# Performance work log

Hardware: AMD Instinct MI355X
Metric: run time of the kernel (lower is better)

Reference implementation:

```python
import jax, jax.numpy as jnp
import numpy as np

N = 50_000          # num_nodes
E = 800_000         # num_edges (avg degree 16)
DIMS = [512, 256, 256, 7]   # embedding_dim
SCALING = 2.0


def _glorot(key, shape):
    lim = float(np.sqrt(6.0 / (shape[0] + shape[1])))
    return jax.random.uniform(key, shape, jnp.float32, -lim, lim)


def setup_inputs() -> dict:
    key = jax.random.key(0)
    ks = jax.random.split(key, 16)
    inp = {
        "x": jax.random.normal(ks[0], (N, DIMS[0]), jnp.float32),
        "edge_index": jax.random.randint(ks[1], (2, E), 0, N, dtype=jnp.int32),
        # GCNConv weights (3 layers)
        "W1": _glorot(ks[2], (DIMS[0], DIMS[1])), "b1": jnp.zeros((DIMS[1],), jnp.float32),
        "W2": _glorot(ks[3], (DIMS[1], DIMS[2])), "b2": jnp.zeros((DIMS[2],), jnp.float32),
        "W3": _glorot(ks[4], (DIMS[2], DIMS[3])), "b3": jnp.zeros((DIMS[3],), jnp.float32),
        # pseudo_mlp: Linear(512,512) -> ReLU -> Linear(512,64) -> ReLU -> Linear(64,out)
        "mw1": _glorot(ks[5], (DIMS[0], 512)), "mb1": jnp.zeros((512,), jnp.float32),
        "mw2": _glorot(ks[6], (512, 64)),      "mb2": jnp.zeros((64,), jnp.float32),
        "mw3": _glorot(ks[7], (64, DIMS[-1])), "mb3": jnp.zeros((DIMS[-1],), jnp.float32),
        # parsing_mats[0] (only index 0 is used: learn_soft_edge3 always called with ln=0)
        "parsing0": jnp.ones((DIMS[-1], DIMS[-1]), jnp.float32) / SCALING,
    }
    return inp


def _gcn_conv(h_in, row, col, edge_weight, W, b):
    """PyG-style GCNConv with self-loops, symmetric norm, and per-edge weights."""
    h = h_in @ W                                  # [N, out]
    loop = jnp.arange(N, dtype=row.dtype)
    r = jnp.concatenate([row, loop])
    c = jnp.concatenate([col, loop])
    ew = jnp.concatenate([edge_weight, jnp.ones((N,), h.dtype)])
    deg = jax.ops.segment_sum(ew, c, num_segments=N)
    dinv = jnp.where(deg > 0, jax.lax.rsqrt(jnp.maximum(deg, 1e-12)), 0.0)
    norm = dinv[r] * ew * dinv[c]                 # [E+N]
    out = jax.ops.segment_sum(h[r] * norm[:, None], c, num_segments=N)
    return out + b


def _learn_soft_edge(x, row, col, mw1, mb1, mw2, mb2, mw3, mb3, parsing0):
    # pseudo_mlp logits
    h = jax.nn.relu(x @ mw1 + mb1)
    h = jax.nn.relu(h @ mw2 + mb2)
    logits = h @ mw3 + mb3                        # [N, C]
    s = logits[row]                               # start_logits [E, C]
    e = logits[col]                               # end_logits   [E, C]
    parsing = jax.nn.relu(SCALING * parsing0)     # [C, C]
    # diag(bmm(outer(s,e), P)).sum(-1) == sum_{c,d} s[e,c] * e[e,d] * P[d,c]
    ew = jnp.sum(s * (e @ parsing), axis=1)       # [E]
    mean = ew.mean()
    var = ew.var(ddof=1)                          # torch .var() is unbiased
    return (ew - mean) * jnp.sqrt(1e-4 / var) + 1.0


def reference(x, edge_index, W1, b1, W2, b2, W3, b3,
              mw1, mb1, mw2, mb2, mw3, mb3, parsing0):
    row, col = edge_index[0], edge_index[1]
    ew = _learn_soft_edge(x, row, col, mw1, mb1, mw2, mb2, mw3, mb3, parsing0)
    # layer 0
    h0 = _gcn_conv(x, row, col, ew, W1, b1)       # h = x (saved, pre-ReLU)
    x1 = jax.nn.relu(h0)                          # dropout is identity in eval
    # layer 1 (+ residual to h0)
    x2 = _gcn_conv(x1, row, col, ew, W2, b2)
    x2 = jax.nn.relu(x2) + h0
    # layer 2 (final, no activation)
    out = _gcn_conv(x2, row, col, ew, W3, b3)     # [N, n_classes]
    return out
```

## Files before the change

### kernel.cpp

```cpp
#include <hip/hip_runtime.h>

#define NN 50000
#define EE 800000
#define NB_EDGE 3125
#define NB_E1   1563
#define NB_SCAN 196

typedef __attribute__((ext_vector_type(4))) float f32x4;
typedef __attribute__((ext_vector_type(8))) short bf16x8;
typedef __attribute__((ext_vector_type(8))) unsigned short u16x8;

typedef const __attribute__((address_space(1))) void* gas_p;
typedef __attribute__((address_space(3))) void* las_p;

__device__ __forceinline__ float bf2f(unsigned short u) {
  union { unsigned int i; float f; } v; v.i = ((unsigned int)u) << 16; return v.f;
}
__device__ __forceinline__ unsigned short f2bf(float f) {
  union { float f; unsigned int i; } v; v.f = f;
  unsigned int u = v.i;
  return (unsigned short)((u + 0x7FFFu + ((u >> 16) & 1u)) >> 16);
}

__device__ __forceinline__ int xcd_swizzle(int orig, int nwg) {
  int xcd = orig & 7;
  int pos = orig >> 3;
  int q = nwg >> 3, r = nwg & 7;
  return (xcd < r ? xcd * (q + 1) : r * (q + 1) + (xcd - r) * q) + pos;
}

constexpr size_t O_XBF  = 0;
constexpr size_t O_H1   = O_XBF + 51200000;
constexpr size_t O_G1   = O_H1  + 51200000;
constexpr size_t O_X1   = O_G1  + 25600000;
constexpr size_t O_H2   = O_X1  + 25600000;
constexpr size_t O_LG   = O_H2  + 6400000;
constexpr size_t O_TG   = O_LG  + 1600000;
constexpr size_t O_EWR  = O_TG  + 1600000;
constexpr size_t O_EWS  = O_EWR + 3200000;
constexpr size_t O_CSR  = O_EWS + 3200000;
constexpr size_t O_MW1T = O_CSR + 6400000;
constexpr size_t O_W1T  = O_MW1T + 524288;
constexpr size_t O_W2T  = O_W1T  + 262144;
constexpr size_t O_MW2T = O_W2T  + 131072;
constexpr size_t O_DEG  = O_MW2T + 65536;
constexpr size_t O_CNT  = O_DEG  + 200192;
constexpr size_t O_CUR  = O_CNT  + 200192;
constexpr size_t O_RED  = O_CUR  + 200192;
constexpr size_t O_RPT  = O_RED  + 256;
constexpr size_t O_DINV = O_RPT  + 200192;
constexpr size_t O_BSUM = O_DINV + 200192;

__global__ __launch_bounds__(256) void conv_f2bf4(const float* __restrict__ in,
                                                  unsigned short* __restrict__ out, int n4) {
  int i = blockIdx.x * 256 + threadIdx.x;
  if (i >= n4) return;
  const float4 v = ((const float4*)in)[i];
  ushort4 o; o.x = f2bf(v.x); o.y = f2bf(v.y); o.z = f2bf(v.z); o.w = f2bf(v.w);
  ((ushort4*)out)[i] = o;
}

__global__ __launch_bounds__(256)
void conv_weights(const float* __restrict__ mw1, const float* __restrict__ W1,
                  const float* __restrict__ W2, const float* __restrict__ mw2,
                  unsigned short* __restrict__ mw1t, unsigned short* __restrict__ w1t,
                  unsigned short* __restrict__ w2t, unsigned short* __restrict__ mw2t)
{
  int i = blockIdx.x * 256 + threadIdx.x;
  if (i < 262144) {
    int k = i >> 9, n = i & 511;
    mw1t[(size_t)n * 512 + k] = f2bf(mw1[i]);
  } else if (i < 393216) {
    int j = i - 262144, k = j >> 8, n = j & 255;
    w1t[(size_t)n * 512 + k] = f2bf(W1[j]);
  } else if (i < 458752) {
    int j = i - 393216, k = j >> 8, n = j & 255;
    w2t[(size_t)n * 256 + k] = f2bf(W2[j]);
  } else if (i < 491520) {
    int j = i - 458752, k = j >> 6, n = j & 63;
    mw2t[(size_t)n * 512 + k] = f2bf(mw2[j]);
  }
}

#define GEMM_STAGE(buf, k0)                                                        \
  _Pragma("unroll")                                                                \
  for (int r = 0; r < 4; ++r) {                                                    \
    const int row = r * 32 + wid * 8 + srow8;                                      \
    int ga = bm + row; ga = ga < M_ ? ga : M_ - 1;                                 \
    int gb = bn + row; gb = gb < N_ ? gb : N_ - 1;                                 \
    __builtin_amdgcn_global_load_lds((gas_p)(pA_ + ((size_t)ga * lda_ + (k0)) * 2 + sks * 16), \
                                     (las_p)(ldsA[buf] + row * 64), 16, 0, 0);     \
    __builtin_amdgcn_global_load_lds((gas_p)(pB_ + ((size_t)gb * ldb_ + (k0)) * 2 + sks * 16), \
                                     (las_p)(ldsB[buf] + row * 64), 16, 0, 0);     \
  }

#define GEMM_BODY(A, lda, Bt, ldb_K, M, Ncols, K, bm, bn)                          \
  __shared__ unsigned short ldsA[2][128 * 64];                                     \
  __shared__ unsigned short ldsB[2][128 * 64];                                     \
  const char* pA_ = (const char*)(A);                                              \
  const char* pB_ = (const char*)(Bt);                                             \
  const int lda_ = (lda), ldb_ = (ldb_K), M_ = (M), N_ = (Ncols);                  \
  const int tid  = threadIdx.x;                                                    \
  const int lane = tid & 63;                                                       \
  const int wid  = tid >> 6;                                                       \
  const int wm   = (wid >> 1) << 6;                                                \
  const int wn   = (wid & 1) << 6;                                                 \
  f32x4 acc[4][4] = {};                                                            \
  const int srow8 = lane >> 3;                                                     \
  const int sks   = (lane & 7) ^ srow8;                                            \
  const int nt    = (K) >> 6;                                                      \
  GEMM_STAGE(0, 0)                                                                 \
  for (int t = 0; t < nt; ++t) {                                                   \
    const int cur = t & 1;                                                         \
    if (t + 1 < nt) {                                                              \
      GEMM_STAGE(cur ^ 1, (t + 1) << 6)                                            \
      asm volatile("s_waitcnt vmcnt(8)" ::: "memory");                             \
    } else {                                                                       \
      asm volatile("s_waitcnt vmcnt(0)" ::: "memory");                             \
    }                                                                              \
    __builtin_amdgcn_s_barrier();                                                  \
    __builtin_amdgcn_sched_barrier(0);                                             \
    const int q   = lane >> 4;                                                     \
    const int r15 = lane & 15;                                                     \
    _Pragma("unroll")                                                              \
    for (int kk = 0; kk < 2; ++kk) {                                               \
      bf16x8 af[4], bfr[4];                                                        \
      _Pragma("unroll")                                                            \
      for (int m = 0; m < 4; ++m) {                                                \
        const int ra = wm + m * 16 + r15;                                          \
        af[m]  = *(const bf16x8*)(ldsA[cur] + ra * 64 + (((kk << 2) + q) ^ (ra & 7)) * 8); \
        const int rb = wn + m * 16 + r15;                                          \
        bfr[m] = *(const bf16x8*)(ldsB[cur] + rb * 64 + (((kk << 2) + q) ^ (rb & 7)) * 8); \
      }                                                                            \
      _Pragma("unroll")                                                            \
      for (int m = 0; m < 4; ++m)                                                  \
        _Pragma("unroll")                                                          \
        for (int n = 0; n < 4; ++n)                                                \
          acc[m][n] = __builtin_amdgcn_mfma_f32_16x16x32_bf16(af[m], bfr[n], acc[m][n], 0, 0, 0); \
    }                                                                              \
    __builtin_amdgcn_sched_barrier(0);                                             \
    __builtin_amdgcn_s_barrier();                                                  \
  }

template<bool RELU, bool BIAS>
__global__ __launch_bounds__(256)
void gemm_bf16(const unsigned short* __restrict__ A, int lda,
               const unsigned short* __restrict__ Bt,
               const float* __restrict__ bias,
               unsigned short* __restrict__ C, int ldc,
               int M, int N, int K)
{
  const int nwg  = gridDim.x * gridDim.y;
  const int wgid = xcd_swizzle(blockIdx.y * gridDim.x + blockIdx.x, nwg);
  const int bn   = (wgid % gridDim.x) << 7;
  const int bm   = (wgid / gridDim.x) << 7;

  GEMM_BODY(A, lda, Bt, K, M, N, K, bm, bn)

  const int q   = lane >> 4;
  const int r15 = lane & 15;
#pragma unroll
  for (int m = 0; m < 4; ++m) {
#pragma unroll
    for (int n = 0; n < 4; ++n) {
      const int gc = bn + wn + n * 16 + r15;
#pragma unroll
      for (int i = 0; i < 4; ++i) {
        const int gr = bm + wm + m * 16 + q * 4 + i;
        if (gr < M && gc < N) {
          float f = acc[m][n][i];
          if (BIAS) f += bias[gc];
          if (RELU) f = fmaxf(f, 0.f);
          C[(size_t)gr * ldc + gc] = f2bf(f);
        }
      }
    }
  }
}

__global__ __launch_bounds__(256)
void gemm_fused(const unsigned short* __restrict__ A,
                const unsigned short* __restrict__ Bt,
                const float* __restrict__ mb1,
                unsigned short* __restrict__ h1,
                unsigned short* __restrict__ g1,
                int M)
{
  const int nwg  = gridDim.x * gridDim.y;
  const int wgid = xcd_swizzle(blockIdx.y * gridDim.x + blockIdx.x, nwg);
  const int bnt  = wgid % gridDim.x;
  const int bn   = bnt << 7;
  const int bm   = (wgid / gridDim.x) << 7;

  GEMM_BODY(A, 512, Bt, 512, M, 768, 512, bm, bn)

  const int q   = lane >> 4;
  const int r15 = lane & 15;
  if (bnt < 4) {
#pragma unroll
    for (int m = 0; m < 4; ++m) {
#pragma unroll
      for (int n = 0; n < 4; ++n) {
        const int gc = bn + wn + n * 16 + r15;
        const float b = mb1[gc];
#pragma unroll
        for (int i = 0; i < 4; ++i) {
          const int gr = bm + wm + m * 16 + q * 4 + i;
          if (gr < M) h1[(size_t)gr * 512 + gc] = f2bf(fmaxf(acc[m][n][i] + b, 0.f));
        }
      }
    }
  } else {
#pragma unroll
    for (int m = 0; m < 4; ++m) {
#pragma unroll
      for (int n = 0; n < 4; ++n) {
        const int gc = bn - 512 + wn + n * 16 + r15;
#pragma unroll
        for (int i = 0; i < 4; ++i) {
          const int gr = bm + wm + m * 16 + q * 4 + i;
          if (gr < M) g1[(size_t)gr * 256 + gc] = f2bf(acc[m][n][i]);
        }
      }
    }
  }
}

__global__ __launch_bounds__(256)
void logits_kernel(const unsigned short* __restrict__ h2, const float* __restrict__ mw3,
                   const float* __restrict__ mb3, const float* __restrict__ par,
                   float* __restrict__ Lg, float* __restrict__ Tg)
{
  __shared__ float w[64 * 8];
  __shared__ float P[64];
  int tid = threadIdx.x;
  for (int i = tid; i < 512; i += 256) {
    int k = i >> 3, c = i & 7;
    w[i] = (c < 7) ? mw3[k * 7 + c] : 0.f;
  }
  if (tid < 64) {
    int d = tid >> 3, c = tid & 7;
    P[tid] = (d < 7 && c < 7) ? fmaxf(2.0f * par[d * 7 + c], 0.f) : 0.f;
  }
  __syncthreads();
  int n = blockIdx.x * 256 + tid;
  if (n >= NN) return;
  const unsigned short* hr = h2 + (size_t)n * 64;
  f32x4 L0 = {0,0,0,0}, L1 = {0,0,0,0};
  for (int k = 0; k < 64; k += 4) {
    ushort4 v = *(const ushort4*)(hr + k);
    float xs[4] = {bf2f(v.x), bf2f(v.y), bf2f(v.z), bf2f(v.w)};
#pragma unroll
    for (int j = 0; j < 4; ++j) {
      L0 += xs[j] * *(const f32x4*)&w[(k + j) * 8];
      L1 += xs[j] * *(const f32x4*)&w[(k + j) * 8 + 4];
    }
  }
  float Ls[8] = {L0[0], L0[1], L0[2], L0[3], L1[0], L1[1], L1[2], 0.f};
#pragma unroll
  for (int c = 0; c < 7; ++c) Ls[c] += mb3[c];
  f32x4 T0 = {0,0,0,0}, T1 = {0,0,0,0};
#pragma unroll
  for (int d = 0; d < 7; ++d) {
    T0 += Ls[d] * *(const f32x4*)&P[d * 8];
    T1 += Ls[d] * *(const f32x4*)&P[d * 8 + 4];
  }
  f32x4 o0 = {Ls[0], Ls[1], Ls[2], Ls[3]};
  f32x4 o1 = {Ls[4], Ls[5], Ls[6], 0.f};
  *(f32x4*)(Lg + (size_t)n * 8)     = o0;
  *(f32x4*)(Lg + (size_t)n * 8 + 4) = o1;
  *(f32x4*)(Tg + (size_t)n * 8)     = T0;
  *(f32x4*)(Tg + (size_t)n * 8 + 4) = T1;
}

__global__ __launch_bounds__(256)
void edge1_kernel(const int* __restrict__ row, const int* __restrict__ col,
                  const float* __restrict__ Lg, const float* __restrict__ Tg,
                  float* __restrict__ ew_raw, int* __restrict__ cnt,
                  double* __restrict__ part)
{
  __shared__ double shs[4], shs2[4];
  const int e0 = blockIdx.x * 512 + threadIdx.x;
  const int e1 = e0 + 256;
  double s = 0.0, s2 = 0.0;
  if (e1 < EE) {
    int r0 = row[e0], c0 = col[e0];
    int r1 = row[e1], c1 = col[e1];
    float4 a00 = *(const float4*)(Lg + (size_t)r0 * 8);
    float4 a01 = *(const float4*)(Lg + (size_t)r0 * 8 + 4);
    float4 a10 = *(const float4*)(Lg + (size_t)r1 * 8);
    float4 a11 = *(const float4*)(Lg + (size_t)r1 * 8 + 4);
    float4 b00 = *(const float4*)(Tg + (size_t)c0 * 8);
    float4 b01 = *(const float4*)(Tg + (size_t)c0 * 8 + 4);
    float4 b10 = *(const float4*)(Tg + (size_t)c1 * 8);
    float4 b11 = *(const float4*)(Tg + (size_t)c1 * 8 + 4);
    float v0 = a00.x*b00.x + a00.y*b00.y + a00.z*b00.z + a00.w*b00.w
             + a01.x*b01.x + a01.y*b01.y + a01.z*b01.z + a01.w*b01.w;
    float v1 = a10.x*b10.x + a10.y*b10.y + a10.z*b10.z + a10.w*b10.w
             + a11.x*b11.x + a11.y*b11.y + a11.z*b11.z + a11.w*b11.w;
    ew_raw[e0] = v0; ew_raw[e1] = v1;
    atomicAdd(&cnt[c0], 1); atomicAdd(&cnt[c1], 1);
    s = (double)v0 + (double)v1;
    s2 = (double)v0 * (double)v0 + (double)v1 * (double)v1;
  } else if (e0 < EE) {
    int r0 = row[e0], c0 = col[e0];
    float4 a00 = *(const float4*)(Lg + (size_t)r0 * 8);
    float4 a01 = *(const float4*)(Lg + (size_t)r0 * 8 + 4);
    float4 b00 = *(const float4*)(Tg + (size_t)c0 * 8);
    float4 b01 = *(const float4*)(Tg + (size_t)c0 * 8 + 4);
    float v0 = a00.x*b00.x + a00.y*b00.y + a00.z*b00.z + a00.w*b00.w
             + a01.x*b01.x + a01.y*b01.y + a01.z*b01.z + a01.w*b01.w;
    ew_raw[e0] = v0;
    atomicAdd(&cnt[c0], 1);
    s = (double)v0; s2 = (double)v0 * (double)v0;
  }
  for (int off = 32; off; off >>= 1) {
    s  += __shfl_down(s, off);
    s2 += __shfl_down(s2, off);
  }
  int wv = threadIdx.x >> 6;
  if ((threadIdx.x & 63) == 0) { shs[wv] = s; shs2[wv] = s2; }
  __syncthreads();
  if (threadIdx.x == 0) {
    part[blockIdx.x]         = shs[0] + shs[1] + shs[2] + shs[3];
    part[NB_E1 + blockIdx.x] = shs2[0] + shs2[1] + shs2[2] + shs2[3];
  }
}

__global__ __launch_bounds__(1024)
void redpart_kernel(const double* __restrict__ part, double* __restrict__ red)
{
  __shared__ double sh[16][2];
  int tid = threadIdx.x;
  double s = 0.0, s2 = 0.0;
  for (int i = tid; i < NB_E1; i += 1024) {
    s  += part[i];
    s2 += part[NB_E1 + i];
  }
  for (int off = 32; off; off >>= 1) {
    s  += __shfl_down(s, off);
    s2 += __shfl_down(s2, off);
  }
  if ((tid & 63) == 0) { sh[tid >> 6][0] = s; sh[tid >> 6][1] = s2; }
  __syncthreads();
  if (tid == 0) {
    double a = 0.0, b = 0.0;
    for (int i = 0; i < 16; ++i) { a += sh[i][0]; b += sh[i][1]; }
    red[0] = a; red[1] = b;
  }
}

__global__ __launch_bounds__(256)
void edge2_kernel(const int* __restrict__ row, const int* __restrict__ col,
                  const float* __restrict__ ew_raw, const double* __restrict__ red,
                  const int* __restrict__ rowptr, int* __restrict__ cursor,
                  float* __restrict__ deg, int2* __restrict__ csr_sw)
{
  int e = blockIdx.x * 256 + threadIdx.x;
  if (e >= EE) return;
  double mean = red[0] / (double)EE;
  double var  = (red[1] - (double)EE * mean * mean) / (double)(EE - 1);
  double scl  = sqrt(1e-4 / var);
  float v = (float)(((double)ew_raw[e] - mean) * scl) + 1.0f;
  int c = col[e];
  atomicAdd(&deg[c], v);
  int pos = atomicAdd(&cursor[c], 1);
  int2 sw; sw.x = row[e]; sw.y = __float_as_int(v);
  csr_sw[rowptr[c] + pos] = sw;
}

__global__ __launch_bounds__(256)
void dinv_kernel(const float* __restrict__ deg, float* __restrict__ dinv)
{
  int n = blockIdx.x * 256 + threadIdx.x;
  if (n >= NN) return;
  float d = deg[n] + 1.0f;
  dinv[n] = d > 0.f ? 1.0f / sqrtf(fmaxf(d, 1e-12f)) : 0.f;
}

__global__ __launch_bounds__(256)
void scan1_kernel(const int* __restrict__ cnt, int* __restrict__ bsum)
{
  __shared__ int sh[4];
  int i = blockIdx.x * 256 + threadIdx.x;
  int v = (i < NN) ? cnt[i] : 0;
  for (int off = 32; off; off >>= 1) v += __shfl_down(v, off);
  if ((threadIdx.x & 63) == 0) sh[threadIdx.x >> 6] = v;
  __syncthreads();
  if (threadIdx.x == 0) bsum[blockIdx.x] = sh[0] + sh[1] + sh[2] + sh[3];
}

__global__ __launch_bounds__(256)
void scan2_kernel(int* __restrict__ bsum)
{
  __shared__ int sh[256];
  int tid = threadIdx.x;
  int v = (tid < NB_SCAN) ? bsum[tid] : 0;
  sh[tid] = v;
  __syncthreads();
  for (int off = 1; off < 256; off <<= 1) {
    int t = (tid >= off) ? sh[tid - off] : 0;
    __syncthreads();
    sh[tid] += t;
    __syncthreads();
  }
  if (tid < NB_SCAN) bsum[tid] = sh[tid] - v;
}

__global__ __launch_bounds__(256)
void scan3_kernel(const int* __restrict__ cnt, const int* __restrict__ bsum,
                  int* __restrict__ rowptr)
{
  __shared__ int sh[256];
  int tid = threadIdx.x;
  int i = blockIdx.x * 256 + tid;
  int v = (i < NN) ? cnt[i] : 0;
  sh[tid] = v;
  __syncthreads();
  for (int off = 1; off < 256; off <<= 1) {
    int t = (tid >= off) ? sh[tid - off] : 0;
    __syncthreads();
    sh[tid] += t;
    __syncthreads();
  }
  if (i < NN) rowptr[i + 1] = bsum[blockIdx.x] + sh[tid];
  if (i == 0) rowptr[0] = 0;
}

#define AGG_ACC(sw_, v_, dv_)                                                \
  {                                                                          \
    float w_ = __int_as_float((sw_).y) * (dv_);                              \
    a0 += w_ * bf2f((v_)[0]); a1 += w_ * bf2f((v_)[1]);                      \
    a2 += w_ * bf2f((v_)[2]); a3 += w_ * bf2f((v_)[3]);                      \
    a4 += w_ * bf2f((v_)[4]); a5 += w_ * bf2f((v_)[5]);                      \
    a6 += w_ * bf2f((v_)[6]); a7 += w_ * bf2f((v_)[7]);                      \
  }

template<int MODE>
__global__ __launch_bounds__(256)
void agg256_kernel(const int* __restrict__ rowptr, const int2* __restrict__ csr_sw,
                   const unsigned short* __restrict__ gsrc,
                   const float* __restrict__ dinv, const float* __restrict__ bias,
                   const unsigned short* __restrict__ h0in,
                   unsigned short* __restrict__ h0out,
                   unsigned short* __restrict__ xout,
                   const float* __restrict__ W3, float* __restrict__ y3)
{
  __shared__ float wlds[2048];
  if (MODE == 1) {
    for (int i = threadIdx.x; i < 2048; i += 256) {
      int c = i & 7;
      wlds[i] = (c < 7) ? W3[(i >> 3) * 7 + c] : 0.f;
    }
    __syncthreads();
  }
  int n = blockIdx.x * 4 + (threadIdx.x >> 6);
  if (n >= NN) return;
  const int lane = threadIdx.x & 63;
  const int half = lane >> 5;
  const int l5   = lane & 31;
  const size_t colbase = (size_t)(l5 << 3);

  float a0=0,a1=0,a2=0,a3=0,a4=0,a5=0,a6=0,a7=0;
  const int s = rowptr[n], e = rowptr[n + 1];
  int i = s + half;
  for (; i + 6 < e; i += 8) {
    int2 sw[4];
#pragma unroll
    for (int u = 0; u < 4; ++u) sw[u] = csr_sw[i + 2 * u];
    float dv[4];
    u16x8 v[4];
#pragma unroll
    for (int u = 0; u < 4; ++u) {
      dv[u] = dinv[sw[u].x];
      v[u]  = *(const u16x8*)(gsrc + (size_t)sw[u].x * 256 + colbase);
    }
#pragma unroll
    for (int u = 0; u < 4; ++u) AGG_ACC(sw[u], v[u], dv[u])
  }
  for (; i < e; i += 2) {
    int2 sw = csr_sw[i];
    float dv = dinv[sw.x];
    u16x8 v = *(const u16x8*)(gsrc + (size_t)sw.x * 256 + colbase);
    AGG_ACC(sw, v, dv)
  }
  a0 += __shfl_xor(a0, 32); a1 += __shfl_xor(a1, 32);
  a2 += __shfl_xor(a2, 32); a3 += __shfl_xor(a3, 32);
  a4 += __shfl_xor(a4, 32); a5 += __shfl_xor(a5, 32);
  a6 += __shfl_xor(a6, 32); a7 += __shfl_xor(a7, 32);
  float f0 = half ? a4 : a0;
  float f1 = half ? a5 : a1;
  float f2 = half ? a6 : a2;
  float f3 = half ? a7 : a3;
  const int dbase = (l5 << 3) + (half << 2);
  const float dn = dinv[n];
  const float wd = dn * dn;
  ushort4 sv = *(const ushort4*)(gsrc + (size_t)n * 256 + dbase);
  float4 b = *(const float4*)(bias + dbase);
  f0 = dn * f0 + wd * bf2f(sv.x) + b.x;
  f1 = dn * f1 + wd * bf2f(sv.y) + b.y;
  f2 = dn * f2 + wd * bf2f(sv.z) + b.z;
  f3 = dn * f3 + wd * bf2f(sv.w) + b.w;
  const size_t o = (size_t)n * 256 + dbase;
  if (MODE == 0) {
    ushort4 h;
    h.x = f2bf(f0); h.y = f2bf(f1); h.z = f2bf(f2); h.w = f2bf(f3);
    *(ushort4*)(h0out + o) = h;
    ushort4 xo;
    xo.x = f2bf(fmaxf(f0, 0.f)); xo.y = f2bf(fmaxf(f1, 0.f));
    xo.z = f2bf(fmaxf(f2, 0.f)); xo.w = f2bf(fmaxf(f3, 0.f));
    *(ushort4*)(xout + o) = xo;
  } else {
    ushort4 h = *(const ushort4*)(h0in + o);
    float x0 = bf2f(f2bf(fmaxf(f0, 0.f) + bf2f(h.x)));
    float x1 = bf2f(f2bf(fmaxf(f1, 0.f) + bf2f(h.y)));
    float x2v = bf2f(f2bf(fmaxf(f2, 0.f) + bf2f(h.z)));
    float x3 = bf2f(f2bf(fmaxf(f3, 0.f) + bf2f(h.w)));
    f32x4 p0 = {0,0,0,0}, p1 = {0,0,0,0};
    p0 += x0 * *(const f32x4*)&wlds[(dbase + 0) * 8];
    p1 += x0 * *(const f32x4*)&wlds[(dbase + 0) * 8 + 4];
    p0 += x1 * *(const f32x4*)&wlds[(dbase + 1) * 8];
    p1 += x1 * *(const f32x4*)&wlds[(dbase + 1) * 8 + 4];
    p0 += x2v * *(const f32x4*)&wlds[(dbase + 2) * 8];
    p1 += x2v * *(const f32x4*)&wlds[(dbase + 2) * 8 + 4];
    p0 += x3 * *(const f32x4*)&wlds[(dbase + 3) * 8];
    p1 += x3 * *(const f32x4*)&wlds[(dbase + 3) * 8 + 4];
#pragma unroll
    for (int off = 1; off < 64; off <<= 1) {
      p0[0] += __shfl_xor(p0[0], off); p0[1] += __shfl_xor(p0[1], off);
      p0[2] += __shfl_xor(p0[2], off); p0[3] += __shfl_xor(p0[3], off);
      p1[0] += __shfl_xor(p1[0], off); p1[1] += __shfl_xor(p1[1], off);
      p1[2] += __shfl_xor(p1[2], off); p1[3] += __shfl_xor(p1[3], off);
    }
    if (lane == 0) {
      *(f32x4*)(y3 + (size_t)n * 8)     = p0;
      *(f32x4*)(y3 + (size_t)n * 8 + 4) = p1;
    }
  }
}

__global__ __launch_bounds__(256)
void agg7_kernel(const int* __restrict__ rowptr, const int2* __restrict__ csr_sw,
                 const float* __restrict__ y3,
                 const float* __restrict__ dinv, const float* __restrict__ b3,
                 float* __restrict__ out)
{
  int n = blockIdx.x * 32 + (threadIdx.x >> 3);
  if (n >= NN) return;
  int j = threadIdx.x & 7;
  float acc = 0.f;
  int s = rowptr[n], e = rowptr[n + 1];
  for (int i = s; i < e; ++i) {
    int2 sw = csr_sw[i];
    acc += __int_as_float(sw.y) * dinv[sw.x] * y3[(size_t)sw.x * 8 + j];
  }
  float dn = dinv[n];
  acc = dn * acc + dn * dn * y3[(size_t)n * 8 + j];
  if (j < 7) out[(size_t)n * 7 + j] = acc + b3[j];
}

extern "C" void kernel_launch(void* const* d_in, const int* in_sizes, int n_in,
                              void* d_out, int out_size, void* d_ws, size_t ws_size,
                              hipStream_t stream)
{
  const float* x   = (const float*)d_in[0];
  const int*   ei  = (const int*)d_in[1];
  const float* W1  = (const float*)d_in[2];
  const float* b1  = (const float*)d_in[3];
  const float* W2  = (const float*)d_in[4];
  const float* b2  = (const float*)d_in[5];
  const float* W3  = (const float*)d_in[6];
  const float* b3  = (const float*)d_in[7];
  const float* mw1 = (const float*)d_in[8];
  const float* mb1 = (const float*)d_in[9];
  const float* mw2 = (const float*)d_in[10];
  const float* mb2 = (const float*)d_in[11];
  const float* mw3 = (const float*)d_in[12];
  const float* mb3 = (const float*)d_in[13];
  const float* par = (const float*)d_in[14];
  const int* row = ei;
  const int* col = ei + EE;
  float* out = (float*)d_out;

  char* ws = (char*)d_ws;
  unsigned short* x_bf  = (unsigned short*)(ws + O_XBF);
  unsigned short* h0    = (unsigned short*)(ws + O_XBF);
  unsigned short* h1_bf = (unsigned short*)(ws + O_H1);
  unsigned short* g2_bf = (unsigned short*)(ws + O_H1);
  unsigned short* g1_bf = (unsigned short*)(ws + O_G1);
  unsigned short* x1_bf = (unsigned short*)(ws + O_X1);
  unsigned short* h2_bf = (unsigned short*)(ws + O_H2);
  float* Lg      = (float*)(ws + O_LG);
  float* Tg      = (float*)(ws + O_TG);
  float* ew_raw  = (float*)(ws + O_EWR);
  float* y3      = (float*)(ws + O_EWR);
  int2*  csr_sw  = (int2*)(ws + O_CSR);
  double* part   = (double*)(ws + O_CSR);
  unsigned short* mw1t = (unsigned short*)(ws + O_MW1T);
  unsigned short* w1t  = (unsigned short*)(ws + O_W1T);
  unsigned short* w2t  = (unsigned short*)(ws + O_W2T);
  unsigned short* mw2t = (unsigned short*)(ws + O_MW2T);
  float*  deg    = (float*)(ws + O_DEG);
  int*    cnt    = (int*)(ws + O_CNT);
  int*    cursor = (int*)(ws + O_CUR);
  double* red    = (double*)(ws + O_RED);
  int*    rowptr = (int*)(ws + O_RPT);
  float*  dinv   = (float*)(ws + O_DINV);
  int*    bsum   = (int*)(ws + O_BSUM);

  hipMemsetAsync(ws + O_DEG, 0, 3 * 200192, stream);

  conv_f2bf4<<<25000, 256, 0, stream>>>(x, x_bf, NN * 512 / 4);
  conv_weights<<<1920, 256, 0, stream>>>(mw1, W1, W2, mw2, mw1t, w1t, w2t, mw2t);

  gemm_fused<<<dim3(6, 391), 256, 0, stream>>>(x_bf, mw1t, mb1, h1_bf, g1_bf, NN);
  gemm_bf16<true,  true ><<<dim3(1, 391), 256, 0, stream>>>(h1_bf, 512, mw2t, mb2, h2_bf, 64, NN, 64, 512);
  logits_kernel<<<196, 256, 0, stream>>>(h2_bf, mw3, mb3, par, Lg, Tg);

  edge1_kernel<<<NB_E1, 256, 0, stream>>>(row, col, Lg, Tg, ew_raw, cnt, part);
  redpart_kernel<<<1, 1024, 0, stream>>>(part, red);
  scan1_kernel<<<NB_SCAN, 256, 0, stream>>>(cnt, bsum);
  scan2_kernel<<<1, 256, 0, stream>>>(bsum);
  scan3_kernel<<<NB_SCAN, 256, 0, stream>>>(cnt, bsum, rowptr);
  edge2_kernel<<<NB_EDGE, 256, 0, stream>>>(row, col, ew_raw, red, rowptr, cursor, deg, csr_sw);
  dinv_kernel<<<196, 256, 0, stream>>>(deg, dinv);

  agg256_kernel<0><<<12500, 256, 0, stream>>>(rowptr, csr_sw, g1_bf, dinv, b1, nullptr, h0, x1_bf, nullptr, nullptr);
  gemm_bf16<false, false><<<dim3(2, 391), 256, 0, stream>>>(x1_bf, 256, w2t, nullptr, g2_bf, 256, NN, 256, 256);
  agg256_kernel<1><<<12500, 256, 0, stream>>>(rowptr, csr_sw, g2_bf, dinv, b2, h0, nullptr, nullptr, W3, y3);
  agg7_kernel<<<1563, 256, 0, stream>>>(rowptr, csr_sw, y3, dinv, b3, out);
}
```

Baseline: 462.7 us.

## Prescale CSR edge weights by source dinv, unroll aggregation deeper, drop W3 LDS staging

Adds a pass that folds dinv[src] into each CSR edge weight once, so the three aggregation kernels no longer gather dinv for every edge. The 256-wide aggregation gains a 16-edge unrolled loop to keep more gathers in flight. W3 is padded to 8 columns once in conv_weights and read straight from global memory, which removes the per-block LDS fill and barrier in mode 1. The cost is one extra kernel launch and an extra read-write pass over the 800K-entry CSR array, plus higher register pressure from the deeper unroll.

```diff
diff --git a/kernel.cpp b/kernel.cpp
--- a/kernel.cpp
+++ b/kernel.cpp
@@ -37,8 +37,8 @@
 constexpr size_t O_LG   = O_H2  + 6400000;
 constexpr size_t O_TG   = O_LG  + 1600000;
 constexpr size_t O_EWR  = O_TG  + 1600000;
-constexpr size_t O_EWS  = O_EWR + 3200000;
-constexpr size_t O_CSR  = O_EWS + 3200000;
+constexpr size_t O_W3P  = O_EWR + 3200000;
+constexpr size_t O_CSR  = O_W3P + 3200000;
 constexpr size_t O_MW1T = O_CSR + 6400000;
 constexpr size_t O_W1T  = O_MW1T + 524288;
 constexpr size_t O_W2T  = O_W1T  + 262144;
@@ -63,8 +63,10 @@
 __global__ __launch_bounds__(256)
 void conv_weights(const float* __restrict__ mw1, const float* __restrict__ W1,
                   const float* __restrict__ W2, const float* __restrict__ mw2,
+                  const float* __restrict__ W3,
                   unsigned short* __restrict__ mw1t, unsigned short* __restrict__ w1t,
-                  unsigned short* __restrict__ w2t, unsigned short* __restrict__ mw2t)
+                  unsigned short* __restrict__ w2t, unsigned short* __restrict__ mw2t,
+                  float* __restrict__ w3p)
 {
   int i = blockIdx.x * 256 + threadIdx.x;
   if (i < 262144) {
@@ -79,6 +81,9 @@
   } else if (i < 491520) {
     int j = i - 458752, k = j >> 6, n = j & 63;
     mw2t[(size_t)n * 512 + k] = f2bf(mw2[j]);
+  } else if (i < 493568) {
+    int j = i - 491520, d = j >> 3, c = j & 7;
+    w3p[j] = (c < 7) ? W3[d * 7 + c] : 0.f;
   }
 }
 
@@ -379,6 +384,16 @@
 }
 
 __global__ __launch_bounds__(256)
+void scale_csr_kernel(int2* __restrict__ csr_sw, const float* __restrict__ dinv)
+{
+  int i = blockIdx.x * 256 + threadIdx.x;
+  if (i >= EE) return;
+  int2 sw = csr_sw[i];
+  sw.y = __float_as_int(__int_as_float(sw.y) * dinv[sw.x]);
+  csr_sw[i] = sw;
+}
+
+__global__ __launch_bounds__(256)
 void scan1_kernel(const int* __restrict__ cnt, int* __restrict__ bsum)
 {
   __shared__ int sh[4];
@@ -427,9 +442,9 @@
   if (i == 0) rowptr[0] = 0;
 }
 
-#define AGG_ACC(sw_, v_, dv_)                                                \
+#define AGG_ACC(sw_, v_)                                                     \
   {                                                                          \
-    float w_ = __int_as_float((sw_).y) * (dv_);                              \
+    float w_ = __int_as_float((sw_).y);                                      \
     a0 += w_ * bf2f((v_)[0]); a1 += w_ * bf2f((v_)[1]);                      \
     a2 += w_ * bf2f((v_)[2]); a3 += w_ * bf2f((v_)[3]);                      \
     a4 += w_ * bf2f((v_)[4]); a5 += w_ * bf2f((v_)[5]);                      \
@@ -444,16 +459,8 @@
                    const unsigned short* __restrict__ h0in,
                    unsigned short* __restrict__ h0out,
                    unsigned short* __restrict__ xout,
-                   const float* __restrict__ W3, float* __restrict__ y3)
-{
-  __shared__ float wlds[2048];
-  if (MODE == 1) {
-    for (int i = threadIdx.x; i < 2048; i += 256) {
-      int c = i & 7;
-      wlds[i] = (c < 7) ? W3[(i >> 3) * 7 + c] : 0.f;
-    }
-    __syncthreads();
-  }
+                   const float* __restrict__ w3p, float* __restrict__ y3)
+{
   int n = blockIdx.x * 4 + (threadIdx.x >> 6);
   if (n >= NN) return;
   const int lane = threadIdx.x & 63;
@@ -464,25 +471,30 @@
   float a0=0,a1=0,a2=0,a3=0,a4=0,a5=0,a6=0,a7=0;
   const int s = rowptr[n], e = rowptr[n + 1];
   int i = s + half;
+  for (; i + 14 < e; i += 16) {
+    int2 sw[8];
+#pragma unroll
+    for (int u = 0; u < 8; ++u) sw[u] = csr_sw[i + 2 * u];
+    u16x8 v[8];
+#pragma unroll
+    for (int u = 0; u < 8; ++u) v[u] = *(const u16x8*)(gsrc + (size_t)sw[u].x * 256 + colbase);
+#pragma unroll
+    for (int u = 0; u < 8; ++u) AGG_ACC(sw[u], v[u])
+  }
   for (; i + 6 < e; i += 8) {
     int2 sw[4];
 #pragma unroll
     for (int u = 0; u < 4; ++u) sw[u] = csr_sw[i + 2 * u];
-    float dv[4];
     u16x8 v[4];
 #pragma unroll
-    for (int u = 0; u < 4; ++u) {
-      dv[u] = dinv[sw[u].x];
-      v[u]  = *(const u16x8*)(gsrc + (size_t)sw[u].x * 256 + colbase);
-    }
-#pragma unroll
-    for (int u = 0; u < 4; ++u) AGG_ACC(sw[u], v[u], dv[u])
+    for (int u = 0; u < 4; ++u) v[u] = *(const u16x8*)(gsrc + (size_t)sw[u].x * 256 + colbase);
+#pragma unroll
+    for (int u = 0; u < 4; ++u) AGG_ACC(sw[u], v[u])
   }
   for (; i < e; i += 2) {
     int2 sw = csr_sw[i];
-    float dv = dinv[sw.x];
     u16x8 v = *(const u16x8*)(gsrc + (size_t)sw.x * 256 + colbase);
-    AGG_ACC(sw, v, dv)
+    AGG_ACC(sw, v)
   }
   a0 += __shfl_xor(a0, 32); a1 += __shfl_xor(a1, 32);
   a2 += __shfl_xor(a2, 32); a3 += __shfl_xor(a3, 32);
@@ -516,15 +528,12 @@
     float x1 = bf2f(f2bf(fmaxf(f1, 0.f) + bf2f(h.y)));
     float x2v = bf2f(f2bf(fmaxf(f2, 0.f) + bf2f(h.z)));
     float x3 = bf2f(f2bf(fmaxf(f3, 0.f) + bf2f(h.w)));
+    const float* w3r = w3p + (size_t)dbase * 8;
     f32x4 p0 = {0,0,0,0}, p1 = {0,0,0,0};
-    p0 += x0 * *(const f32x4*)&wlds[(dbase + 0) * 8];
-    p1 += x0 * *(const f32x4*)&wlds[(dbase + 0) * 8 + 4];
-    p0 += x1 * *(const f32x4*)&wlds[(dbase + 1) * 8];
-    p1 += x1 * *(const f32x4*)&wlds[(dbase + 1) * 8 + 4];
-    p0 += x2v * *(const f32x4*)&wlds[(dbase + 2) * 8];
-    p1 += x2v * *(const f32x4*)&wlds[(dbase + 2) * 8 + 4];
-    p0 += x3 * *(const f32x4*)&wlds[(dbase + 3) * 8];
-    p1 += x3 * *(const f32x4*)&wlds[(dbase + 3) * 8 + 4];
+    p0 += x0 * *(const f32x4*)(w3r +  0); p1 += x0 * *(const f32x4*)(w3r +  4);
+    p0 += x1 * *(const f32x4*)(w3r +  8); p1 += x1 * *(const f32x4*)(w3r + 12);
+    p0 += x2v * *(const f32x4*)(w3r + 16); p1 += x2v * *(const f32x4*)(w3r + 20);
+    p0 += x3 * *(const f32x4*)(w3r + 24); p1 += x3 * *(const f32x4*)(w3r + 28);
 #pragma unroll
     for (int off = 1; off < 64; off <<= 1) {
       p0[0] += __shfl_xor(p0[0], off); p0[1] += __shfl_xor(p0[1], off);
@@ -552,7 +561,7 @@
   int s = rowptr[n], e = rowptr[n + 1];
   for (int i = s; i < e; ++i) {
     int2 sw = csr_sw[i];
-    acc += __int_as_float(sw.y) * dinv[sw.x] * y3[(size_t)sw.x * 8 + j];
+    acc += __int_as_float(sw.y) * y3[(size_t)sw.x * 8 + j];
   }
   float dn = dinv[n];
   acc = dn * acc + dn * dn * y3[(size_t)n * 8 + j];
@@ -594,6 +603,7 @@
   float* Tg      = (float*)(ws + O_TG);
   float* ew_raw  = (float*)(ws + O_EWR);
   float* y3      = (float*)(ws + O_EWR);
+  float* w3p     = (float*)(ws + O_W3P);
   int2*  csr_sw  = (int2*)(ws + O_CSR);
   double* part   = (double*)(ws + O_CSR);
   unsigned short* mw1t = (unsigned short*)(ws + O_MW1T);
@@ -611,7 +621,7 @@
   hipMemsetAsync(ws + O_DEG, 0, 3 * 200192, stream);
 
   conv_f2bf4<<<25000, 256, 0, stream>>>(x, x_bf, NN * 512 / 4);
-  conv_weights<<<1920, 256, 0, stream>>>(mw1, W1, W2, mw2, mw1t, w1t, w2t, mw2t);
+  conv_weights<<<1929, 256, 0, stream>>>(mw1, W1, W2, mw2, W3, mw1t, w1t, w2t, mw2t, w3p);
 
   gemm_fused<<<dim3(6, 391), 256, 0, stream>>>(x_bf, mw1t, mb1, h1_bf, g1_bf, NN);
   gemm_bf16<true,  true ><<<dim3(1, 391), 256, 0, stream>>>(h1_bf, 512, mw2t, mb2, h2_bf, 64, NN, 64, 512);
@@ -624,9 +634,10 @@
   scan3_kernel<<<NB_SCAN, 256, 0, stream>>>(cnt, bsum, rowptr);
   edge2_kernel<<<NB_EDGE, 256, 0, stream>>>(row, col, ew_raw, red, rowptr, cursor, deg, csr_sw);
   dinv_kernel<<<196, 256, 0, stream>>>(deg, dinv);
+  scale_csr_kernel<<<NB_EDGE, 256, 0, stream>>>(csr_sw, dinv);
 
   agg256_kernel<0><<<12500, 256, 0, stream>>>(rowptr, csr_sw, g1_bf, dinv, b1, nullptr, h0, x1_bf, nullptr, nullptr);
   gemm_bf16<false, false><<<dim3(2, 391), 256, 0, stream>>>(x1_bf, 256, w2t, nullptr, g2_bf, 256, NN, 256, 256);
-  agg256_kernel<1><<<12500, 256, 0, stream>>>(rowptr, csr_sw, g2_bf, dinv, b2, h0, nullptr, nullptr, W3, y3);
+  agg256_kernel<1><<<12500, 256, 0, stream>>>(rowptr, csr_sw, g2_bf, dinv, b2, h0, nullptr, nullptr, w3p, y3);
   agg7_kernel<<<1563, 256, 0, stream>>>(rowptr, csr_sw, y3, dinv, b3, out);
 }
```

Measured after the change: 459.6 us. No clear change (-0.7%).
